# Kernel tuning notes

Measured on AMD Instinct MI355X. Metric: run time of the kernel, lower is better.

The kernel has to match this reference:

```python
import jax, jax.numpy as jnp
import numpy as np

DIM = 1024
HEADS = 16
DIM_HEAD = 64
SCALE = DIM_HEAD ** -0.5
LN_EPS = 1e-5


def layer_norm(x, g, b):
    mu = jnp.mean(x, axis=-1, keepdims=True)
    var = jnp.mean(jnp.square(x - mu), axis=-1, keepdims=True)
    return (x - mu) * jax.lax.rsqrt(var + LN_EPS) * g + b


def setup_inputs() -> dict:
    key = jax.random.key(0)
    ks = jax.random.split(key, 8)
    w_std = DIM ** -0.5  # keep GEMM outputs O(1)
    return {
        "query": jax.random.normal(ks[0], (4, 512, DIM), jnp.float32),
        "kv": jax.random.normal(ks[1], (4, 2048, DIM), jnp.float32),
        "ln_q_g": jnp.ones((DIM,), jnp.float32),
        "ln_q_b": jnp.zeros((DIM,), jnp.float32),
        "ln_kv_g": jnp.ones((DIM,), jnp.float32),
        "ln_kv_b": jnp.zeros((DIM,), jnp.float32),
        "Wq": jax.random.normal(ks[2], (DIM, DIM), jnp.float32) * w_std,
        "bq": jnp.zeros((DIM,), jnp.float32),
        "Wk": jax.random.normal(ks[3], (DIM, DIM), jnp.float32) * w_std,
        "bk": jnp.zeros((DIM,), jnp.float32),
        "Wv": jax.random.normal(ks[4], (DIM, DIM), jnp.float32) * w_std,
        "bv": jnp.zeros((DIM,), jnp.float32),
        "Wo": jax.random.normal(ks[5], (DIM, DIM), jnp.float32) * w_std,
        "bo": jnp.zeros((DIM,), jnp.float32),
    }


def reference(query, kv, ln_q_g, ln_q_b, ln_kv_g, ln_kv_b,
              Wq, bq, Wk, bk, Wv, bv, Wo, bo):
    kv_n = layer_norm(kv, ln_kv_g, ln_kv_b)            # (b, n_kv, d)
    residual = query
    q_n = layer_norm(query, ln_q_g, ln_q_b)            # (b, n_q, d)

    q = q_n @ Wq + bq                                   # (b, n_q, inner)
    kv_input = jnp.concatenate((kv_n, q_n), axis=-2)    # (b, n_kv+n_q, d)
    k = kv_input @ Wk + bk
    v = kv_input @ Wv + bv

    def split_heads(t):
        b, n, _ = t.shape
        return t.reshape(b, n, HEADS, DIM_HEAD).transpose(0, 2, 1, 3)  # b h n dh

    q = split_heads(q) * SCALE
    k = split_heads(k)
    v = split_heads(v)

    sim = jnp.einsum('bhid,bhjd->bhij', q, k)           # (b, h, n_q, n_kv+n_q)
    sim = sim - jax.lax.stop_gradient(jnp.max(sim, axis=-1, keepdims=True))
    attn = jax.nn.softmax(sim, axis=-1)
    out = jnp.einsum('bhij,bhjd->bhid', attn, v)        # (b, h, n_q, dh)

    b, h, n, dh = out.shape
    out = out.transpose(0, 2, 1, 3).reshape(b, n, h * dh)
    return out @ Wo + bo + residual
```

## Files before the change

### kernel.cpp

```cpp
#include <hip/hip_runtime.h>
#include <hip/hip_bf16.h>

#define B_    4
#define NQ    512
#define NKV   2048
#define NT    2560
#define DIM_  1024
#define HEADS 16
#define DH    64
#define NSEQT 10240
#define SCALE_Q_L2E 0.18033688011112042f

typedef short bf16x8 __attribute__((ext_vector_type(8)));
typedef float f32x4  __attribute__((ext_vector_type(4)));
typedef __hip_bfloat16 bf16;

__device__ inline void gll16(const bf16* g, bf16* l) {
  __builtin_amdgcn_global_load_lds(
      (const __attribute__((address_space(1))) unsigned int*)g,
      (__attribute__((address_space(3))) unsigned int*)l, 16, 0, 0);
}

#define VMCNT(n) asm volatile("s_waitcnt vmcnt(" #n ")" ::: "memory")
#define BAR() __builtin_amdgcn_s_barrier()

__global__ __launch_bounds__(256) void prep_kernel(
    const float* __restrict__ query, const float* __restrict__ kv,
    const float* __restrict__ lgq, const float* __restrict__ lbq,
    const float* __restrict__ lgkv, const float* __restrict__ lbkv,
    bf16* __restrict__ X,
    const float* __restrict__ W0, const float* __restrict__ W1,
    const float* __restrict__ W2, const float* __restrict__ W3,
    bf16* __restrict__ T0, bf16* __restrict__ T1,
    bf16* __restrict__ T2, bf16* __restrict__ T3)
{
  __shared__ __align__(16) char psm[9216];
  const int t = threadIdx.x;
  const int blkid = blockIdx.x;
  if (blkid < B_*NT) {
    float* sh = (float*)psm;
    int b = blkid / NT, r = blkid % NT;
    const float *src, *g, *bb;
    if (r < NKV) { src = kv    + ((size_t)b*NKV + r)*DIM_;      g = lgkv; bb = lbkv; }
    else         { src = query + ((size_t)b*NQ + (r-NKV))*DIM_; g = lgq;  bb = lbq;  }
    float4 v = ((const float4*)src)[t];
    float s  = v.x+v.y+v.z+v.w;
    float s2 = v.x*v.x+v.y*v.y+v.z*v.z+v.w*v.w;
    #pragma unroll
    for (int m=1;m<64;m<<=1){ s += __shfl_xor(s,m,64); s2 += __shfl_xor(s2,m,64); }
    int wave=t>>6, lane=t&63;
    if(lane==0){ sh[wave]=s; sh[4+wave]=s2; }
    __syncthreads();
    s  = sh[0]+sh[1]+sh[2]+sh[3];
    s2 = sh[4]+sh[5]+sh[6]+sh[7];
    float mu = s*(1.0f/DIM_);
    float rs = rsqrtf(s2*(1.0f/DIM_) - mu*mu + 1e-5f);
    float4 gg = ((const float4*)g)[t];
    float4 b4 = ((const float4*)bb)[t];
    bf16* dst = X + (size_t)blkid*DIM_ + t*4;
    dst[0]=__float2bfloat16((v.x-mu)*rs*gg.x + b4.x);
    dst[1]=__float2bfloat16((v.y-mu)*rs*gg.y + b4.y);
    dst[2]=__float2bfloat16((v.z-mu)*rs*gg.z + b4.z);
    dst[3]=__float2bfloat16((v.w-mu)*rs*gg.w + b4.w);
  } else {
    int l = blkid - B_*NT;
    const float* W; bf16* Wt;
    switch (l>>8) {
      case 0: W=W0; Wt=T0; break;
      case 1: W=W1; Wt=T1; break;
      case 2: W=W2; Wt=T2; break;
      default: W=W3; Wt=T3; break;
    }
    int rem = l & 255;
    int k0 = (rem&15)*64, n0 = (rem>>4)*64;
    bf16* Ws = (bf16*)psm;
    int kr = t>>2, nseg = (t&3)*16;
    const float4* s4 = (const float4*)(W + (size_t)(k0+kr)*DIM_ + n0 + nseg);
    union { uint4 u[2]; bf16 h[16]; } pk;
    #pragma unroll
    for (int j=0;j<4;j++){
      float4 v = s4[j];
      pk.h[j*4+0]=__float2bfloat16(v.x); pk.h[j*4+1]=__float2bfloat16(v.y);
      pk.h[j*4+2]=__float2bfloat16(v.z); pk.h[j*4+3]=__float2bfloat16(v.w);
    }
    *(uint4*)(Ws + kr*72 + nseg)     = pk.u[0];
    *(uint4*)(Ws + kr*72 + nseg + 8) = pk.u[1];
    __syncthreads();
    int n = t&63, kseg = t>>6;
    union { uint4 u[2]; bf16 h[16]; } o;
    #pragma unroll
    for (int k=0;k<16;k++) o.h[k] = Ws[(kseg*16+k)*72 + n];
    bf16* dst = Wt + (size_t)(n0+n)*DIM_ + k0 + kseg*16;
    *(uint4*)dst = o.u[0];
    *(uint4*)(dst+8) = o.u[1];
  }
}

__device__ __forceinline__ void gemm_core2(
    const bf16* __restrict__ A, const bf16* __restrict__ Bmat,
    const float* __restrict__ bias, const float* __restrict__ residual,
    void* __restrict__ outv, int rows_per_batch, int row_offset,
    int a_batch_stride_rows, int n_seq, float scale,
    int emode, int m0, int n0, char* smem)
{
  char* const sA = smem;
  char* const sB = smem + 32768;
  float* Ts = (float*)smem;

  const int t = threadIdx.x;
  const int srow = t >> 3;
  const int gsw  = (t & 7) ^ (srow & 7);
  const bf16* pA[4]; const bf16* pB[4];
  #pragma unroll
  for (int c = 0; c < 4; ++c) {
    int gm = m0 + c*32 + srow;
    int bi = gm / rows_per_batch;
    pA[c] = A + ((size_t)bi*a_batch_stride_rows + row_offset
                 + (gm - bi*rows_per_batch))*(size_t)DIM_ + gsw*8;
    pB[c] = Bmat + (size_t)(n0 + c*32 + srow)*(size_t)DIM_ + gsw*8;
  }
  const int toff = t*16;

  const int wave = t>>6, lane = t&63, qq = lane>>4, mr = lane&15;
  const int wm = (wave>>1)*64, wn = (wave&1)*64;
  const int xq0 = (( qq    ) ^ (mr&7)) << 4;
  const int xq1 = ((4 + qq ) ^ (mr&7)) << 4;

  f32x4 acc[4][4] = {};

  #pragma unroll
  for (int c=0;c<4;++c) gll16(pA[c], (bf16*)(sA + c*4096 + toff));
  #pragma unroll
  for (int c=0;c<4;++c) gll16(pB[c], (bf16*)(sB + c*4096 + toff));
  VMCNT(0);
  BAR();

  for (int kt = 0; kt < 16; ++kt) {
    const int cb = (kt&1) << 14;
    const int nb = ((kt+1)&1) << 14;
    if (kt < 15) {
      const int ko = (kt+1)*64;
      #pragma unroll
      for (int c=0;c<4;++c) gll16(pA[c] + ko, (bf16*)(sA + nb + c*4096 + toff));
      #pragma unroll
      for (int c=0;c<4;++c) gll16(pB[c] + ko, (bf16*)(sB + nb + c*4096 + toff));
    }
    #pragma unroll
    for (int kh = 0; kh < 2; ++kh) {
      const int xq = kh ? xq1 : xq0;
      bf16x8 af[4], bfr[4];
      #pragma unroll
      for (int ms=0; ms<4; ++ms)
        af[ms]  = *(const bf16x8*)(sA + cb + (wm + ms*16 + mr)*128 + xq);
      #pragma unroll
      for (int ns=0; ns<4; ++ns)
        bfr[ns] = *(const bf16x8*)(sB + cb + (wn + ns*16 + mr)*128 + xq);
      __builtin_amdgcn_s_setprio(1);
      #pragma unroll
      for (int ms=0; ms<4; ++ms)
        #pragma unroll
        for (int ns=0; ns<4; ++ns)
          acc[ms][ns] = __builtin_amdgcn_mfma_f32_16x16x32_bf16(
              af[ms], bfr[ns], acc[ms][ns], 0,0,0);
      __builtin_amdgcn_s_setprio(0);
    }
    VMCNT(0);
    BAR();
  }
  __syncthreads();

  const int lr = t>>3, cs = (t&7)*16;
  for (int R=0; R<4; R++){
    if ((wave>>1) == (R>>1)) {
      #pragma unroll
      for (int ms2=0; ms2<2; ms2++){
        int ms = (R&1)*2 + ms2;
        #pragma unroll
        for (int ns=0; ns<4; ns++){
          int col = wn + ns*16 + mr;
          #pragma unroll
          for (int r=0;r<4;r++)
            Ts[(ms2*16 + qq*4 + r)*132 + col] = acc[ms][ns][r];
        }
      }
    }
    __syncthreads();
    float v[16];
    #pragma unroll
    for (int j=0;j<4;j++){
      float4 f = *(const float4*)(Ts + lr*132 + cs + j*4);
      v[j*4+0]=f.x; v[j*4+1]=f.y; v[j*4+2]=f.z; v[j*4+3]=f.w;
    }
    int gr = m0 + R*32 + lr;
    int gc = n0 + cs;
    if (emode == 0) {
      float* out = (float*)outv;
      size_t base = (size_t)gr*DIM_ + gc;
      #pragma unroll
      for (int j=0;j<4;j++){
        float4 bv = *(const float4*)(bias + gc + j*4);
        float4 rv = *(const float4*)(residual + base + j*4);
        float4 o4;
        o4.x = v[j*4+0] + bv.x + rv.x;
        o4.y = v[j*4+1] + bv.y + rv.y;
        o4.z = v[j*4+2] + bv.z + rv.z;
        o4.w = v[j*4+3] + bv.w + rv.w;
        *(float4*)(out + base + j*4) = o4;
      }
    } else if (emode == 1) {
      int bb = gr / rows_per_batch;
      int n  = gr - bb*rows_per_batch;
      int hh = gc>>6, dh = gc&63;
      bf16* out = (bf16*)outv + ((size_t)(bb*HEADS + hh)*n_seq + n)*DH + dh;
      union { uint4 u[2]; bf16 h[16]; } pk;
      #pragma unroll
      for (int j=0;j<16;j++) pk.h[j] = __float2bfloat16((v[j] + bias[gc+j])*scale);
      *(uint4*)out     = pk.u[0];
      *(uint4*)(out+8) = pk.u[1];
    } else {
      float bc = bias[gr];
      bf16* out = (bf16*)outv + (size_t)gr*NSEQT + gc;
      union { uint4 u[2]; bf16 h[16]; } pk;
      #pragma unroll
      for (int j=0;j<16;j++) pk.h[j] = __float2bfloat16(v[j] + bc);
      *(uint4*)out     = pk.u[0];
      *(uint4*)(out+8) = pk.u[1];
    }
    __syncthreads();
  }
}

__global__ __launch_bounds__(256) void gemm_qkv3(
    const bf16* __restrict__ X,
    const bf16* __restrict__ WtQ, const bf16* __restrict__ WtK,
    const bf16* __restrict__ WtV,
    const float* __restrict__ bq, const float* __restrict__ bk,
    const float* __restrict__ bv,
    bf16* __restrict__ Qhb, bf16* __restrict__ Khb, bf16* __restrict__ VTg)
{
  __shared__ __align__(16) char smem[65536];
  const int blk = blockIdx.x;
  if (blk < 128) {
    gemm_core2(X, WtQ, bq, nullptr, Qhb, NQ, NKV, NT, NQ, SCALE_Q_L2E, 1,
               (blk&15)*128, (blk>>4)*128, smem);
  } else if (blk < 768) {
    int l = blk - 128;
    gemm_core2(X, WtK, bk, nullptr, Khb, NT, 0, NT, NT, 1.0f, 1,
               (l%80)*128, (l/80)*128, smem);
  } else {
    int l = blk - 768;
    gemm_core2(WtV, X, bv, nullptr, VTg, DIM_, 0, DIM_, NSEQT, 1.0f, 2,
               (l/80)*128, (l%80)*128, smem);
  }
}

__global__ __launch_bounds__(256) void gemm_o(
    const bf16* __restrict__ Ctx, const bf16* __restrict__ WtO,
    const float* __restrict__ bo, const float* __restrict__ residual,
    float* __restrict__ out)
{
  __shared__ __align__(16) char smem[65536];
  const int blk = blockIdx.x;
  gemm_core2(Ctx, WtO, bo, residual, out, B_*NQ, 0, B_*NQ, NQ, 1.0f, 0,
             (blk&15)*128, (blk>>4)*128, smem);
}

__global__ __launch_bounds__(256) void attn6_kernel(
    const bf16* __restrict__ Qh, const bf16* __restrict__ Kh,
    const bf16* __restrict__ VTg, bf16* __restrict__ Ctx)
{
  __shared__ __align__(16) bf16 KV[2][8192];
  __shared__ __align__(16) unsigned int Ps[4][640];

  const int t = threadIdx.x, wave = t>>6, lane = t&63;
  const int qq = lane>>4, mr = lane&15;
  const int blk = blockIdx.x;
  const int bh = (blk&7)*8 + (blk>>6);
  const int q0 = ((blk>>3)&7)*64;
  const int b = bh>>4, h = bh&15;
  const int pair = wave>>1, kh = wave&1;
  const int qb = pair*32;

  const int sl = t>>2, sc = t&3;
  const int skey = 32*(sl>>5) + 2*(sl&15) + ((sl>>4)&1);
  const bf16* Kb  = Kh + (size_t)bh*NT*DH + (size_t)skey*DH + sc*8;
  const bf16* VbT = VTg + ((size_t)(h*DH) + sl)*NSEQT + (size_t)b*NT + sc*8;

  bf16x8 qf[2][2];
  #pragma unroll
  for (int mt=0; mt<2; mt++){
    const bf16* Qb = Qh + ((size_t)bh*NQ + q0 + qb + mt*16 + mr)*DH;
    qf[mt][0] = *(const bf16x8*)(Qb + qq*8);
    qf[mt][1] = *(const bf16x8*)(Qb + 32 + qq*8);
  }

  f32x4 o[2][4] = {};
  float l[2][4] = {};
  unsigned int* Pw = &Ps[wave][0];

  {
    bf16* bp = &KV[0][0];
    gll16(Kb,        bp + t*8);
    gll16(Kb + 32,   bp + 2048 + t*8);
    gll16(VbT,       bp + 4096 + t*8);
    gll16(VbT + 32,  bp + 6144 + t*8);
  }

  for (int it = 0; it < NT/64; it++) {
    __syncthreads();
    if (it + 1 < NT/64) {
      int kt = (it+1)*64;
      bf16* bp = &KV[(it+1)&1][0];
      gll16(Kb  + (size_t)kt*DH,      bp + t*8);
      gll16(Kb  + (size_t)kt*DH + 32, bp + 2048 + t*8);
      gll16(VbT + kt,                 bp + 4096 + t*8);
      gll16(VbT + kt + 32,            bp + 6144 + t*8);
    }
    const bf16* cbuf = &KV[it&1][0];

    bf16x8 kf[2][2];
    #pragma unroll
    for (int g=0; g<2; g++){
      kf[g][0] = *(const bf16x8*)(cbuf + (32*kh + 16*g + mr)*32 + qq*8);
      kf[g][1] = *(const bf16x8*)(cbuf + 2048 + (32*kh + 16*g + mr)*32 + qq*8);
    }
    f32x4 s[2][2];
    #pragma unroll
    for (int mt=0; mt<2; mt++)
      #pragma unroll
      for (int g=0; g<2; g++){
        f32x4 z = {};
        z = __builtin_amdgcn_mfma_f32_16x16x32_bf16(qf[mt][0], kf[g][0], z, 0,0,0);
        z = __builtin_amdgcn_mfma_f32_16x16x32_bf16(qf[mt][1], kf[g][1], z, 0,0,0);
        s[mt][g] = z;
      }
    bf16x8 vf[4];
    #pragma unroll
    for (int n2=0; n2<4; n2++)
      vf[n2] = *(const bf16x8*)(cbuf + 4096 + kh*2048 + (n2*16+mr)*32 + qq*8);

    #pragma unroll
    for (int mt=0; mt<2; mt++)
      #pragma unroll
      for (int r=0; r<4; r++){
        float e0 = __builtin_amdgcn_exp2f(s[mt][0][r]);
        float e1 = __builtin_amdgcn_exp2f(s[mt][1][r]);
        l[mt][r] += e0 + e1;
        unsigned a0 = __float_as_uint(e0) + 0x8000u;
        unsigned a1 = __float_as_uint(e1) + 0x8000u;
        Pw[(mt*16 + qq*4 + r)*20 + mr] = __builtin_amdgcn_perm(a1, a0, 0x07060302u);
      }
    asm volatile("s_waitcnt lgkmcnt(0)" ::: "memory");
    bf16x8 pa[2];
    #pragma unroll
    for (int mt=0; mt<2; mt++)
      pa[mt] = *(const bf16x8*)(Pw + (mt*16+mr)*20 + qq*4);
    #pragma unroll
    for (int mt=0; mt<2; mt++)
      #pragma unroll
      for (int n2=0; n2<4; n2++)
        o[mt][n2] = __builtin_amdgcn_mfma_f32_16x16x32_bf16(pa[mt], vf[n2], o[mt][n2], 0,0,0);
  }

  float lsum[2][4];
  #pragma unroll
  for (int mt=0; mt<2; mt++)
    #pragma unroll
    for (int r=0; r<4; r++){
      float v = l[mt][r];
      #pragma unroll
      for (int m=1;m<16;m<<=1) v += __shfl_xor(v, m, 16);
      lsum[mt][r] = v;
    }

  __syncthreads();
  float* Of  = (float*)&KV[0][0];
  float* lsh = (float*)&Ps[0][0];
  if (kh == 1) {
    #pragma unroll
    for (int mt=0; mt<2; mt++){
      #pragma unroll
      for (int n2=0; n2<4; n2++)
        #pragma unroll
        for (int r=0; r<4; r++)
          Of[(qb + mt*16 + qq*4 + r)*68 + n2*16 + mr] = o[mt][n2][r];
      if (mr == 0)
        #pragma unroll
        for (int r=0; r<4; r++)
          lsh[qb + mt*16 + qq*4 + r] = lsum[mt][r];
    }
  }
  __syncthreads();
  if (kh == 0) {
    #pragma unroll
    for (int mt=0; mt<2; mt++)
      #pragma unroll
      for (int r=0; r<4; r++){
        int row = qb + mt*16 + qq*4 + r;
        float rl = 1.0f / (lsum[mt][r] + lsh[row]);
        #pragma unroll
        for (int n2=0; n2<4; n2++){
          int idx = row*68 + n2*16 + mr;
          Of[idx] = (o[mt][n2][r] + Of[idx]) * rl;
        }
      }
  }
  __syncthreads();
  {
    int row = t>>2, seg = (t&3)*16;
    union { uint4 u[2]; bf16 hh[16]; } pkv;
    #pragma unroll
    for (int j=0;j<16;j++) pkv.hh[j] = __float2bfloat16(Of[row*68 + seg + j]);
    bf16* dst = Ctx + ((size_t)b*NQ + q0 + row)*DIM_ + h*DH + seg;
    *(uint4*)dst = pkv.u[0];
    *(uint4*)(dst+8) = pkv.u[1];
  }
}

extern "C" void kernel_launch(void* const* d_in, const int* in_sizes, int n_in,
                              void* d_out, int out_size, void* d_ws, size_t ws_size,
                              hipStream_t stream)
{
  const float* query  = (const float*)d_in[0];
  const float* kv     = (const float*)d_in[1];
  const float* ln_q_g = (const float*)d_in[2];
  const float* ln_q_b = (const float*)d_in[3];
  const float* ln_kv_g= (const float*)d_in[4];
  const float* ln_kv_b= (const float*)d_in[5];
  const float* Wq = (const float*)d_in[6];
  const float* bq = (const float*)d_in[7];
  const float* Wk = (const float*)d_in[8];
  const float* bk = (const float*)d_in[9];
  const float* Wv = (const float*)d_in[10];
  const float* bv = (const float*)d_in[11];
  const float* Wo = (const float*)d_in[12];
  const float* bo = (const float*)d_in[13];
  float* out = (float*)d_out;

  char* ws = (char*)d_ws;
  size_t off = 0;
  auto take = [&](size_t bytes)->char* {
    char* p = ws + off; off += (bytes + 255) & ~(size_t)255; return p;
  };
  bf16* X    = (bf16*)take((size_t)B_*NT*DIM_*2);
  bf16* Qhb  = (bf16*)take((size_t)B_*NQ*DIM_*2);
  bf16* Khb  = (bf16*)take((size_t)B_*NT*DIM_*2);
  bf16* VTg  = (bf16*)take((size_t)DIM_*NSEQT*2);
  bf16* Ctx  = (bf16*)take((size_t)B_*NQ*DIM_*2);
  bf16* WtQ  = (bf16*)take((size_t)DIM_*DIM_*2);
  bf16* WtK  = (bf16*)take((size_t)DIM_*DIM_*2);
  bf16* WtV  = (bf16*)take((size_t)DIM_*DIM_*2);
  bf16* WtO  = (bf16*)take((size_t)DIM_*DIM_*2);

  prep_kernel<<<B_*NT + 1024, 256, 0, stream>>>(
      query, kv, ln_q_g, ln_q_b, ln_kv_g, ln_kv_b, X,
      Wq, Wk, Wv, Wo, WtQ, WtK, WtV, WtO);

  gemm_qkv3<<<1408, 256, 0, stream>>>(X, WtQ, WtK, WtV, bq, bk, bv,
                                      Qhb, Khb, VTg);

  attn6_kernel<<<512, 256, 0, stream>>>(Qhb, Khb, VTg, Ctx);

  gemm_o<<<128, 256, 0, stream>>>(Ctx, WtO, bo, query, out);
}
```

Measured before the change: 234.0 us.

## Triple-buffer attention K/V loads with vmcnt waits and MFMA priority hints

Moves the attention kernel's K/V staging from a double buffer to a triple buffer in shared memory. Loads run two tiles ahead, and the wait is a partial vmcnt before a raw barrier instead of a full __syncthreads, so more global latency overlaps with compute. s_setprio is raised around the MFMA blocks to favour matrix work across waves. The cost is more LDS per block (48KB of KV), which may lower occupancy, and redundant clamped loads on the last iterations.

```diff
diff --git a/kernel.cpp b/kernel.cpp
--- a/kernel.cpp
+++ b/kernel.cpp
@@ -265,11 +265,11 @@
              (blk&15)*128, (blk>>4)*128, smem);
 }
 
-__global__ __launch_bounds__(256) void attn6_kernel(
+__global__ __launch_bounds__(256) void attn7_kernel(
     const bf16* __restrict__ Qh, const bf16* __restrict__ Kh,
     const bf16* __restrict__ VTg, bf16* __restrict__ Ctx)
 {
-  __shared__ __align__(16) bf16 KV[2][8192];
+  __shared__ __align__(16) bf16 KV[3][8192];
   __shared__ __align__(16) unsigned int Ps[4][640];
 
   const int t = threadIdx.x, wave = t>>6, lane = t&63;
@@ -298,25 +298,31 @@
   float l[2][4] = {};
   unsigned int* Pw = &Ps[wave][0];
 
-  {
-    bf16* bp = &KV[0][0];
-    gll16(Kb,        bp + t*8);
-    gll16(Kb + 32,   bp + 2048 + t*8);
-    gll16(VbT,       bp + 4096 + t*8);
-    gll16(VbT + 32,  bp + 6144 + t*8);
-  }
-
-  for (int it = 0; it < NT/64; it++) {
-    __syncthreads();
-    if (it + 1 < NT/64) {
-      int kt = (it+1)*64;
-      bf16* bp = &KV[(it+1)&1][0];
-      gll16(Kb  + (size_t)kt*DH,      bp + t*8);
-      gll16(Kb  + (size_t)kt*DH + 32, bp + 2048 + t*8);
-      gll16(VbT + kt,                 bp + 4096 + t*8);
-      gll16(VbT + kt + 32,            bp + 6144 + t*8);
-    }
-    const bf16* cbuf = &KV[it&1][0];
+  const int NIT = NT/64;
+
+  #pragma unroll
+  for (int p = 0; p < 2; ++p) {
+    bf16* bp = &KV[p][0];
+    const size_t kt = (size_t)p*64;
+    gll16(Kb  + kt*DH,      bp + t*8);
+    gll16(Kb  + kt*DH + 32, bp + 2048 + t*8);
+    gll16(VbT + kt,         bp + 4096 + t*8);
+    gll16(VbT + kt + 32,    bp + 6144 + t*8);
+  }
+
+  for (int it = 0; it < NIT; it++) {
+    VMCNT(4);
+    BAR();
+    {
+      int pt = (it + 2 <= NIT - 1) ? (it + 2) : (NIT - 1);
+      size_t kt = (size_t)pt*64;
+      bf16* bp = &KV[(it+2)%3][0];
+      gll16(Kb  + kt*DH,      bp + t*8);
+      gll16(Kb  + kt*DH + 32, bp + 2048 + t*8);
+      gll16(VbT + kt,         bp + 4096 + t*8);
+      gll16(VbT + kt + 32,    bp + 6144 + t*8);
+    }
+    const bf16* cbuf = &KV[it%3][0];
 
     bf16x8 kf[2][2];
     #pragma unroll
@@ -325,6 +331,7 @@
       kf[g][1] = *(const bf16x8*)(cbuf + 2048 + (32*kh + 16*g + mr)*32 + qq*8);
     }
     f32x4 s[2][2];
+    __builtin_amdgcn_s_setprio(1);
     #pragma unroll
     for (int mt=0; mt<2; mt++)
       #pragma unroll
@@ -334,6 +341,7 @@
         z = __builtin_amdgcn_mfma_f32_16x16x32_bf16(qf[mt][1], kf[g][1], z, 0,0,0);
         s[mt][g] = z;
       }
+    __builtin_amdgcn_s_setprio(0);
     bf16x8 vf[4];
     #pragma unroll
     for (int n2=0; n2<4; n2++)
@@ -355,11 +363,13 @@
     #pragma unroll
     for (int mt=0; mt<2; mt++)
       pa[mt] = *(const bf16x8*)(Pw + (mt*16+mr)*20 + qq*4);
+    __builtin_amdgcn_s_setprio(1);
     #pragma unroll
     for (int mt=0; mt<2; mt++)
       #pragma unroll
       for (int n2=0; n2<4; n2++)
         o[mt][n2] = __builtin_amdgcn_mfma_f32_16x16x32_bf16(pa[mt], vf[n2], o[mt][n2], 0,0,0);
+    __builtin_amdgcn_s_setprio(0);
   }
 
   float lsum[2][4];
@@ -459,7 +469,7 @@
   gemm_qkv3<<<1408, 256, 0, stream>>>(X, WtQ, WtK, WtV, bq, bk, bv,
                                       Qhb, Khb, VTg);
 
-  attn6_kernel<<<512, 256, 0, stream>>>(Qhb, Khb, VTg, Ctx);
+  attn7_kernel<<<512, 256, 0, stream>>>(Qhb, Khb, VTg, Ctx);
 
   gemm_o<<<128, 256, 0, stream>>>(Ctx, WtO, bo, query, out);
 }
```

Result: slower. 238.8 us (+2.0%).

## Use triple-buffered K=32 GEMM pipeline and one-wave-per-row LayerNorm

Applied to the files above, without the earlier changes.

The shared GEMM core moves from a double-buffered K=64 loop to a triple-buffered K=32 loop that prefetches two stages ahead with a partial vmcnt wait. This cuts LDS use to 48KB so three blocks can share a CU, aiming to hide global-load latency better. The LayerNorm prep now gives one row to each wave, dropping the cross-wave barrier and writing packed 8-byte stores. The cost is twice as many barriers per K step and a redundant final prefetch issued at the clamped last tile.

```diff
diff --git a/kernel.cpp b/kernel.cpp
--- a/kernel.cpp
+++ b/kernel.cpp
@@ -24,7 +24,7 @@
 #define VMCNT(n) asm volatile("s_waitcnt vmcnt(" #n ")" ::: "memory")
 #define BAR() __builtin_amdgcn_s_barrier()
 
-__global__ __launch_bounds__(256) void prep_kernel(
+__global__ __launch_bounds__(256) void prep2_kernel(
     const float* __restrict__ query, const float* __restrict__ kv,
     const float* __restrict__ lgq, const float* __restrict__ lbq,
     const float* __restrict__ lgkv, const float* __restrict__ lbkv,
@@ -37,33 +37,40 @@
   __shared__ __align__(16) char psm[9216];
   const int t = threadIdx.x;
   const int blkid = blockIdx.x;
-  if (blkid < B_*NT) {
-    float* sh = (float*)psm;
-    int b = blkid / NT, r = blkid % NT;
-    const float *src, *g, *bb;
-    if (r < NKV) { src = kv    + ((size_t)b*NKV + r)*DIM_;      g = lgkv; bb = lbkv; }
-    else         { src = query + ((size_t)b*NQ + (r-NKV))*DIM_; g = lgq;  bb = lbq;  }
-    float4 v = ((const float4*)src)[t];
-    float s  = v.x+v.y+v.z+v.w;
-    float s2 = v.x*v.x+v.y*v.y+v.z*v.z+v.w*v.w;
+  if (blkid < 2560) {
+    const int w = t>>6, l = t&63;
+    const int R = blkid*4 + w;
+    int b = R / NT, r = R % NT;
+    const float *src, *gp, *bp;
+    if (r < NKV) { src = kv    + ((size_t)b*NKV + r)*DIM_;      gp = lgkv; bp = lbkv; }
+    else         { src = query + ((size_t)b*NQ + (r-NKV))*DIM_; gp = lgq;  bp = lbq;  }
+    float4 v[4];
+    #pragma unroll
+    for (int j=0;j<4;++j) v[j] = ((const float4*)src)[j*64 + l];
+    float s = 0.f, s2 = 0.f;
+    #pragma unroll
+    for (int j=0;j<4;++j){
+      s  += v[j].x+v[j].y+v[j].z+v[j].w;
+      s2 += v[j].x*v[j].x+v[j].y*v[j].y+v[j].z*v[j].z+v[j].w*v[j].w;
+    }
     #pragma unroll
     for (int m=1;m<64;m<<=1){ s += __shfl_xor(s,m,64); s2 += __shfl_xor(s2,m,64); }
-    int wave=t>>6, lane=t&63;
-    if(lane==0){ sh[wave]=s; sh[4+wave]=s2; }
-    __syncthreads();
-    s  = sh[0]+sh[1]+sh[2]+sh[3];
-    s2 = sh[4]+sh[5]+sh[6]+sh[7];
     float mu = s*(1.0f/DIM_);
     float rs = rsqrtf(s2*(1.0f/DIM_) - mu*mu + 1e-5f);
-    float4 gg = ((const float4*)g)[t];
-    float4 b4 = ((const float4*)bb)[t];
-    bf16* dst = X + (size_t)blkid*DIM_ + t*4;
-    dst[0]=__float2bfloat16((v.x-mu)*rs*gg.x + b4.x);
-    dst[1]=__float2bfloat16((v.y-mu)*rs*gg.y + b4.y);
-    dst[2]=__float2bfloat16((v.z-mu)*rs*gg.z + b4.z);
-    dst[3]=__float2bfloat16((v.w-mu)*rs*gg.w + b4.w);
+    uint2* drow = (uint2*)(X + (size_t)R*DIM_);
+    #pragma unroll
+    for (int j=0;j<4;++j){
+      float4 gg = ((const float4*)gp)[j*64 + l];
+      float4 b4 = ((const float4*)bp)[j*64 + l];
+      union { unsigned int u[2]; bf16 h[4]; } pk;
+      pk.h[0] = __float2bfloat16((v[j].x-mu)*rs*gg.x + b4.x);
+      pk.h[1] = __float2bfloat16((v[j].y-mu)*rs*gg.y + b4.y);
+      pk.h[2] = __float2bfloat16((v[j].z-mu)*rs*gg.z + b4.z);
+      pk.h[3] = __float2bfloat16((v[j].w-mu)*rs*gg.w + b4.w);
+      drow[j*64 + l] = make_uint2(pk.u[0], pk.u[1]);
+    }
   } else {
-    int l = blkid - B_*NT;
+    int l = blkid - 2560;
     const float* W; bf16* Wt;
     switch (l>>8) {
       case 0: W=W0; Wt=T0; break;
@@ -96,7 +103,7 @@
   }
 }
 
-__device__ __forceinline__ void gemm_core2(
+__device__ __forceinline__ void gemm_core3(
     const bf16* __restrict__ A, const bf16* __restrict__ Bmat,
     const float* __restrict__ bias, const float* __restrict__ residual,
     void* __restrict__ outv, int rows_per_batch, int row_offset,
@@ -104,57 +111,61 @@
     int emode, int m0, int n0, char* smem)
 {
   char* const sA = smem;
-  char* const sB = smem + 32768;
+  char* const sB = smem + 24576;
   float* Ts = (float*)smem;
 
   const int t = threadIdx.x;
-  const int srow = t >> 3;
-  const int gsw  = (t & 7) ^ (srow & 7);
-  const bf16* pA[4]; const bf16* pB[4];
+  const int lrow = t>>3, sl = t&7;
+  const int sp   = sl ^ (lrow & 7);
+  const int hsel = sp>>2, g = sp&3;
+  const bf16 *pA[2], *pB[2];
   #pragma unroll
-  for (int c = 0; c < 4; ++c) {
-    int gm = m0 + c*32 + srow;
+  for (int c = 0; c < 2; ++c) {
+    int gm = m0 + 32*c + lrow + 64*hsel;
     int bi = gm / rows_per_batch;
     pA[c] = A + ((size_t)bi*a_batch_stride_rows + row_offset
-                 + (gm - bi*rows_per_batch))*(size_t)DIM_ + gsw*8;
-    pB[c] = Bmat + (size_t)(n0 + c*32 + srow)*(size_t)DIM_ + gsw*8;
+                 + (gm - bi*rows_per_batch))*(size_t)DIM_ + g*8;
+    int gn = n0 + 32*c + lrow + 64*hsel;
+    pB[c] = Bmat + (size_t)gn*(size_t)DIM_ + g*8;
   }
   const int toff = t*16;
 
   const int wave = t>>6, lane = t&63, qq = lane>>4, mr = lane&15;
   const int wm = (wave>>1)*64, wn = (wave&1)*64;
-  const int xq0 = (( qq    ) ^ (mr&7)) << 4;
-  const int xq1 = ((4 + qq ) ^ (mr&7)) << 4;
+  const int sAo = ((((wm>>6)<<2)|qq) ^ (mr&7))*16 + mr*128;
+  const int sBo = ((((wn>>6)<<2)|qq) ^ (mr&7))*16 + mr*128;
 
   f32x4 acc[4][4] = {};
 
   #pragma unroll
-  for (int c=0;c<4;++c) gll16(pA[c], (bf16*)(sA + c*4096 + toff));
-  #pragma unroll
-  for (int c=0;c<4;++c) gll16(pB[c], (bf16*)(sB + c*4096 + toff));
-  VMCNT(0);
-  BAR();
-
-  for (int kt = 0; kt < 16; ++kt) {
-    const int cb = (kt&1) << 14;
-    const int nb = ((kt+1)&1) << 14;
-    if (kt < 15) {
-      const int ko = (kt+1)*64;
-      #pragma unroll
-      for (int c=0;c<4;++c) gll16(pA[c] + ko, (bf16*)(sA + nb + c*4096 + toff));
-      #pragma unroll
-      for (int c=0;c<4;++c) gll16(pB[c] + ko, (bf16*)(sB + nb + c*4096 + toff));
-    }
-    #pragma unroll
-    for (int kh = 0; kh < 2; ++kh) {
-      const int xq = kh ? xq1 : xq0;
+  for (int p = 0; p < 2; ++p) {
+    const int ko = p*32, bo = p*8192;
+    gll16(pA[0]+ko, (bf16*)(sA + bo + toff));
+    gll16(pA[1]+ko, (bf16*)(sA + bo + 4096 + toff));
+    gll16(pB[0]+ko, (bf16*)(sB + bo + toff));
+    gll16(pB[1]+ko, (bf16*)(sB + bo + 4096 + toff));
+  }
+
+  int rd = 0, wr2 = 2;
+  for (int kt = 0; kt < 32; ++kt) {
+    {
+      const int kt2 = (kt+2 < 32) ? kt+2 : 31;
+      const int ko = kt2*32, bo = wr2*8192;
+      gll16(pA[0]+ko, (bf16*)(sA + bo + toff));
+      gll16(pA[1]+ko, (bf16*)(sA + bo + 4096 + toff));
+      gll16(pB[0]+ko, (bf16*)(sB + bo + toff));
+      gll16(pB[1]+ko, (bf16*)(sB + bo + 4096 + toff));
+    }
+    VMCNT(8);
+    BAR();
+    {
+      const char* Ab = sA + rd*8192;
+      const char* Bb = sB + rd*8192;
       bf16x8 af[4], bfr[4];
       #pragma unroll
-      for (int ms=0; ms<4; ++ms)
-        af[ms]  = *(const bf16x8*)(sA + cb + (wm + ms*16 + mr)*128 + xq);
-      #pragma unroll
-      for (int ns=0; ns<4; ++ns)
-        bfr[ns] = *(const bf16x8*)(sB + cb + (wn + ns*16 + mr)*128 + xq);
+      for (int ms=0; ms<4; ++ms) af[ms]  = *(const bf16x8*)(Ab + ms*2048 + sAo);
+      #pragma unroll
+      for (int ns=0; ns<4; ++ns) bfr[ns] = *(const bf16x8*)(Bb + ns*2048 + sBo);
       __builtin_amdgcn_s_setprio(1);
       #pragma unroll
       for (int ms=0; ms<4; ++ms)
@@ -164,9 +175,11 @@
               af[ms], bfr[ns], acc[ms][ns], 0,0,0);
       __builtin_amdgcn_s_setprio(0);
     }
-    VMCNT(0);
     BAR();
-  }
+    rd  = (rd  == 2) ? 0 : rd  + 1;
+    wr2 = (wr2 == 2) ? 0 : wr2 + 1;
+  }
+  VMCNT(0);
   __syncthreads();
 
   const int lr = t>>3, cs = (t&7)*16;
@@ -230,7 +243,7 @@
   }
 }
 
-__global__ __launch_bounds__(256) void gemm_qkv3(
+__global__ __launch_bounds__(256, 3) void gemm_qkv4(
     const bf16* __restrict__ X,
     const bf16* __restrict__ WtQ, const bf16* __restrict__ WtK,
     const bf16* __restrict__ WtV,
@@ -238,30 +251,30 @@
     const float* __restrict__ bv,
     bf16* __restrict__ Qhb, bf16* __restrict__ Khb, bf16* __restrict__ VTg)
 {
-  __shared__ __align__(16) char smem[65536];
+  __shared__ __align__(16) char smem[49152];
   const int blk = blockIdx.x;
   if (blk < 128) {
-    gemm_core2(X, WtQ, bq, nullptr, Qhb, NQ, NKV, NT, NQ, SCALE_Q_L2E, 1,
+    gemm_core3(X, WtQ, bq, nullptr, Qhb, NQ, NKV, NT, NQ, SCALE_Q_L2E, 1,
                (blk&15)*128, (blk>>4)*128, smem);
   } else if (blk < 768) {
     int l = blk - 128;
-    gemm_core2(X, WtK, bk, nullptr, Khb, NT, 0, NT, NT, 1.0f, 1,
+    gemm_core3(X, WtK, bk, nullptr, Khb, NT, 0, NT, NT, 1.0f, 1,
                (l%80)*128, (l/80)*128, smem);
   } else {
     int l = blk - 768;
-    gemm_core2(WtV, X, bv, nullptr, VTg, DIM_, 0, DIM_, NSEQT, 1.0f, 2,
+    gemm_core3(WtV, X, bv, nullptr, VTg, DIM_, 0, DIM_, NSEQT, 1.0f, 2,
                (l/80)*128, (l%80)*128, smem);
   }
 }
 
-__global__ __launch_bounds__(256) void gemm_o(
+__global__ __launch_bounds__(256, 3) void gemm_o(
     const bf16* __restrict__ Ctx, const bf16* __restrict__ WtO,
     const float* __restrict__ bo, const float* __restrict__ residual,
     float* __restrict__ out)
 {
-  __shared__ __align__(16) char smem[65536];
+  __shared__ __align__(16) char smem[49152];
   const int blk = blockIdx.x;
-  gemm_core2(Ctx, WtO, bo, residual, out, B_*NQ, 0, B_*NQ, NQ, 1.0f, 0,
+  gemm_core3(Ctx, WtO, bo, residual, out, B_*NQ, 0, B_*NQ, NQ, 1.0f, 0,
              (blk&15)*128, (blk>>4)*128, smem);
 }
 
@@ -452,11 +465,11 @@
   bf16* WtV  = (bf16*)take((size_t)DIM_*DIM_*2);
   bf16* WtO  = (bf16*)take((size_t)DIM_*DIM_*2);
 
-  prep_kernel<<<B_*NT + 1024, 256, 0, stream>>>(
+  prep2_kernel<<<3584, 256, 0, stream>>>(
       query, kv, ln_q_g, ln_q_b, ln_kv_g, ln_kv_b, X,
       Wq, Wk, Wv, Wo, WtQ, WtK, WtV, WtO);
 
-  gemm_qkv3<<<1408, 256, 0, stream>>>(X, WtQ, WtK, WtV, bq, bk, bv,
+  gemm_qkv4<<<1408, 256, 0, stream>>>(X, WtQ, WtK, WtV, bq, bk, bv,
                                       Qhb, Khb, VTg);
 
   attn6_kernel<<<512, 256, 0, stream>>>(Qhb, Khb, VTg, Ctx);
```

New measurement: 240.0 us. +2.5%, slower.
